# Kernel optimization log

Measured on AMD Instinct MI355X. Metric: run time of the kernel, lower is better.

Reference implementation:

```python
import jax, jax.numpy as jnp
import numpy as np

B, N_SIDE, S = 64, 40, 512
N = N_SIDE * N_SIDE          # 1600 grid points (fl_feature_dims [1,40,40])
EMB = 10                     # embedding_dim
GDIM = 8                     # lie('homography').dim
WIDTH = 128
C1 = 20                      # first-layer output channels


def _embed(x, emb_dim):
    # sinusoidal embedding of each scalar coordinate: [..., D] -> [..., D*emb_dim]
    freqs = 2.0 ** jnp.arange(emb_dim // 2, dtype=x.dtype)
    ang = x[..., None] * freqs                       # [..., D, emb/2]
    e = jnp.concatenate([jnp.sin(ang), jnp.cos(ang)], axis=-1)  # [..., D, emb]
    return e.reshape(x.shape[:-1] + (x.shape[-1] * emb_dim,))


def _glorot(key, shape):
    fan_in = shape[0]
    return jax.random.normal(key, shape, dtype=jnp.float32) / np.sqrt(fan_in)


def setup_inputs() -> dict:
    key = jax.random.key(0)
    ks = jax.random.split(key, 16)
    inp = {
        'data':   jax.random.normal(ks[0], (B, N, 1), dtype=jnp.float32),
        'v0':     jax.random.normal(ks[1], (S, GDIM), dtype=jnp.float32),
        'v_last': jax.random.normal(ks[2], (S, GDIM), dtype=jnp.float32),
        # FirstLayer filter MLP: 2*EMB -> 20 -> 20 -> 1*C1
        'fl_w1': _glorot(ks[3], (2 * EMB, 20)), 'fl_b1': jnp.zeros((20,), jnp.float32),
        'fl_w2': _glorot(ks[4], (20, 20)),      'fl_b2': jnp.zeros((20,), jnp.float32),
        'fl_w3': _glorot(ks[5], (20, C1)),      'fl_b3': jnp.zeros((C1,), jnp.float32),
        # Hidden FilterMLP: EMB*GDIM=80 -> WIDTH -> C1*WIDTH
        's_w1': _glorot(ks[6], (EMB * GDIM, WIDTH)), 's_b1': jnp.zeros((WIDTH,), jnp.float32),
        's_w2': _glorot(ks[7], (WIDTH, C1 * WIDTH)), 's_b2': jnp.zeros((C1 * WIDTH,), jnp.float32),
        'fc1_w': _glorot(ks[8], (WIDTH, WIDTH)), 'fc1_b': jnp.zeros((WIDTH,), jnp.float32),
        'fc2_w': _glorot(ks[9], (WIDTH, WIDTH)), 'fc2_b': jnp.zeros((WIDTH,), jnp.float32),
        'pool_w': _glorot(ks[10], (WIDTH, 10)),  'pool_b': jnp.zeros((10,), jnp.float32),
    }
    return inp


def reference(data, v0, v_last, fl_w1, fl_b1, fl_w2, fl_b2, fl_w3, fl_b3,
              s_w1, s_b1, s_w2, s_b2, fc1_w, fc1_b, fc2_w, fc2_b, pool_w, pool_b):
    silu = jax.nn.silu
    # pixel grid in [-1,1]^2, homogeneous coords [N,3]
    lin = jnp.linspace(-1.0, 1.0, N_SIDE, dtype=data.dtype)
    xx, yy = jnp.meshgrid(lin, lin, indexing='ij')
    coords = jnp.stack([xx.ravel(), yy.ravel()], axis=-1)           # [N,2]
    xh = jnp.concatenate([coords, jnp.ones((N, 1), data.dtype)], -1)  # [N,3]
    # homography matrices: identity + small perturbation from 8 group params
    pert = jnp.concatenate([0.1 * v_last, jnp.zeros((S, 1), data.dtype)], -1).reshape(S, 3, 3)
    H = jnp.eye(3, dtype=data.dtype) + pert                          # [S,3,3]
    y = jnp.einsum('sij,nj->sni', H, xh)                             # [S,N,3]
    t = y[..., :2] / y[..., 2:3]                                     # projective action [S,N,2]
    # continuous-kernel first layer: filters generated by MLP on embedded coords
    e1 = _embed(t, EMB)                                              # [S,N,20]
    h = silu(e1 @ fl_w1 + fl_b1)
    h = silu(h @ fl_w2 + fl_b2)
    filt1 = h @ fl_w3 + fl_b3                                        # [S,N,C1]
    z = jnp.einsum('bn,sno->bso', data[:, :, 0], filt1) / N          # [B,S,C1]
    z = silu(z)
    # hidden FilterMLP on group samples v0 -> per-sample filters [S,C1,WIDTH]
    v0e = _embed(v0, EMB)                                            # [S,80]
    h2 = silu(v0e @ s_w1 + s_b1)                                     # [S,WIDTH]
    filt2 = (h2 @ s_w2 + s_b2).reshape(S, C1, WIDTH)
    # (1/S) * sum over group-sample and channel axes of broadcast product
    z = jnp.einsum('bsc,scw->bw', z, filt2) / S                      # [B,WIDTH]
    z = silu(z @ fc1_w + fc1_b) + z
    z = silu(z @ fc2_w + fc2_b) + z
    return z @ pool_w + pool_b                                       # [B,10]
```

## Files before the change

kernel.cpp:

```cpp
#include <hip/hip_runtime.h>

#define N_PTS 1600
#define NSIDE 40
#define SNUM  512
#define BNUM  64
#define C1D   20
#define WID   128

typedef _Float16 h8  __attribute__((ext_vector_type(8)));
typedef _Float16 h4  __attribute__((ext_vector_type(4)));
typedef __fp16   h2v __attribute__((ext_vector_type(2)));
typedef float    f4  __attribute__((ext_vector_type(4)));

__device__ __forceinline__ float silu_f(float x){
    return x * __builtin_amdgcn_rcpf(1.f + __expf(-x));
}
__device__ __forceinline__ void fma4(float4& a, float s, const float4 w){
    a.x += s*w.x; a.y += s*w.y; a.z += s*w.z; a.w += s*w.w;
}

__global__ __launch_bounds__(256) void ka_prep(
    const float* __restrict__ data, const float* __restrict__ v0,
    const float* __restrict__ s_w1, const float* __restrict__ s_b1,
    const float* __restrict__ s_w2, const float* __restrict__ s_b2,
    const float* __restrict__ w1, const float* __restrict__ b1,
    const float* __restrict__ w2, const float* __restrict__ b2,
    const float* __restrict__ w3, const float* __restrict__ b3,
    _Float16* __restrict__ dataA, float* __restrict__ f2g,
    _Float16* __restrict__ wPackA, float* __restrict__ bPackA,
    float* __restrict__ out2g)
{
    const int t  = threadIdx.x;
    const int bx = blockIdx.x;
    if (bx == 370) {
        const float* wsrc[3] = { w1, w2, w3 };
        const float* bsrc[3] = { b1, b2, b3 };
        for (int v = t; v < 3072; v += 256) {
            const int l = v >> 10, rem = v & 1023;
            const int cout = rem >> 5, cin = rem & 31;
            float x = 0.f;
            if (cout < 20 && cin < 20) x = wsrc[l][cin * 20 + cout];
            wPackA[v] = (_Float16)x;
        }
        if (t < 96) {
            const int l = t >> 5, cout = t & 31;
            bPackA[t] = (cout < 20) ? bsrc[l][cout] : 0.f;
        }
        for (int v = t; v < 8192; v += 256) out2g[v] = 0.f;
        return;
    }
    if (bx >= 320) {
        const int o  = (bx - 320) * 256 + t;
        const int L  = o & 63, cm = o >> 6;
        const int mt = cm & 3, ch = cm >> 2;
        const int b  = mt * 16 + (L & 15);
        const int nb = ch * 32 + (L >> 4) * 8;
        const float* src = data + b * N_PTS + nb;
        h8 v;
        #pragma unroll
        for (int j = 0; j < 8; j++) v[j] = (_Float16)src[j];
        *(h8*)(dataA + (size_t)o * 8) = v;
        return;
    }
    const int st  = bx / 10, ct = bx - st * 10;
    const int s0  = st * 16;
    const int col = ct * 256 + t;
    __shared__ __align__(16) float h2t[128][20];

    for (int idx = t; idx < 2048; idx += 256) {
        const int ss = idx >> 7, j = idx & 127;
        float acc = s_b1[j];
        #pragma unroll
        for (int d = 0; d < 8; d++) {
            const float val = v0[(s0 + ss) * 8 + d];
            float sv, cv;
            __sincosf(val, &sv, &cv);
            #pragma unroll
            for (int k = 0; k < 5; k++) {
                acc += sv * s_w1[(d*10 + k)     * WID + j];
                acc += cv * s_w1[(d*10 + 5 + k) * WID + j];
                const float ns = 2.f * sv * cv;
                const float nc = 1.f - 2.f * sv * sv;
                sv = ns; cv = nc;
            }
        }
        h2t[j][ss] = silu_f(acc);
    }
    __syncthreads();

    float4 acc[4];
    #pragma unroll
    for (int qq = 0; qq < 4; qq++) acc[qq] = make_float4(0.f, 0.f, 0.f, 0.f);
    #pragma unroll 4
    for (int i = 0; i < 128; i++) {
        const float wv = s_w2[i * 2560 + col];
        const float4* hh = (const float4*)&h2t[i][0];
        #pragma unroll
        for (int qq = 0; qq < 4; qq++) fma4(acc[qq], wv, hh[qq]);
    }
    const float bias = s_b2[col];
    const float* af = (const float*)acc;
    #pragma unroll
    for (int ss = 0; ss < 16; ss++)
        f2g[(s0 + ss) * 2560 + col] = af[ss] + bias;
}

__device__ __forceinline__ void embed_pt(int n, const float Hm[9], h2v e2[10])
{
    const int i = n / NSIDE;
    const int j = n - i * NSIDE;
    const float x = -1.f + (float)i * (2.f/39.f);
    const float y = -1.f + (float)j * (2.f/39.f);
    const float y0 = Hm[0]*x + Hm[1]*y + Hm[2];
    const float y1 = Hm[3]*x + Hm[4]*y + Hm[5];
    const float y2 = Hm[6]*x + Hm[7]*y + Hm[8];
    const float inv = __builtin_amdgcn_rcpf(y2);
    const float t0 = y0 * inv, t1 = y1 * inv;
    float e[20];
    float sv0, cv0, sv1, cv1;
    __sincosf(t0, &sv0, &cv0);
    __sincosf(t1, &sv1, &cv1);
    #pragma unroll
    for (int k = 0; k < 5; k++) {
        e[k] = sv0; e[5+k] = cv0; e[10+k] = sv1; e[15+k] = cv1;
        const float ns0 = 2.f*sv0*cv0, nc0 = 1.f - 2.f*sv0*sv0; sv0 = ns0; cv0 = nc0;
        const float ns1 = 2.f*sv1*cv1, nc1 = 1.f - 2.f*sv1*sv1; sv1 = ns1; cv1 = nc1;
    }
    #pragma unroll
    for (int k = 0; k < 10; k++)
        e2[k] = __builtin_amdgcn_cvt_pkrtz(e[2*k], e[2*k+1]);
}

#define ASTRIDE 40

__global__ __launch_bounds__(512, 8) void k1_filt_z(
    const _Float16* __restrict__ dataA, const float* __restrict__ v_last,
    const _Float16* __restrict__ wPackA, const float* __restrict__ bPackA,
    float* __restrict__ zpart)
{
    const int s    = blockIdx.x & 511;
    const int half = blockIdx.x >> 9;
    const int nb0  = half * 800;
    const int t    = threadIdx.x;
    const int lane = t & 63;
    const int w    = t >> 6;
    const int q    = lane >> 4;
    const int l15  = lane & 15;
    const int mtbase = (w & 1) * 2;
    const int kcs    = w >> 1;

    __shared__ __align__(16) unsigned char pool[21504];
    __shared__ __align__(16) _Float16 filtB[20 * 264];
    __shared__ __align__(16) _Float16 wlds[3072];
    __shared__ __align__(16) float    blds[96];
    _Float16* act = (_Float16*)pool;
    float*    red = (float*)pool;

    for (int v = t; v < 1536; v += 512)
        ((unsigned int*)wlds)[v] = ((const unsigned int*)wPackA)[v];
    if (t < 96) blds[t] = bPackA[t];

    float Hm[9];
    #pragma unroll
    for (int k = 0; k < 9; k++) Hm[k] = (k == 0 || k == 4 || k == 8) ? 1.f : 0.f;
    #pragma unroll
    for (int k = 0; k < 8; k++) Hm[k] += 0.1f * v_last[s*8 + k];

    f4 zacc[2][2];
    #pragma unroll
    for (int mi = 0; mi < 2; mi++) { zacc[mi][0] = (f4)(0.f); zacc[mi][1] = (f4)(0.f); }
    const f4 zero4 = (f4)(0.f);

    if (t < 256) {
        unsigned long long* pz = (unsigned long long*)(act + t*ASTRIDE + 20);
        pz[0] = 0ull; pz[1] = 0ull; pz[2] = 0ull;
    }

    for (int base = 0; base < 800; base += 256) {
        const int tn = min(256, 800 - base);
        if (t < tn) {
            h2v e2[10];
            embed_pt(nb0 + base + t, Hm, e2);
            #pragma unroll
            for (int k = 0; k < 10; k++)
                *(h2v*)(act + t*ASTRIDE + 2*k) = e2[k];
        }
        __syncthreads();

        const int nmt = tn >> 4;
        #pragma unroll
        for (int l = 0; l < 3; l++) {
            const h8 wf0 = *(const h8*)(wlds + ((l*2+0)*16 + l15) * 32 + q*8);
            const h8 wf1 = *(const h8*)(wlds + ((l*2+1)*16 + l15) * 32 + q*8);
            const float b0 = blds[(l*2+0)*16 + l15];
            const float b1 = blds[(l*2+1)*16 + l15];
            for (int mt = w; mt < nmt; mt += 8) {
                const int r0 = mt * 16;
                const h8 af = *(const h8*)(act + (r0 + l15)*ASTRIDE + q*8);
                f4 D0 = __builtin_amdgcn_mfma_f32_16x16x32_f16(af, wf0, zero4, 0, 0, 0);
                f4 D1 = __builtin_amdgcn_mfma_f32_16x16x32_f16(af, wf1, zero4, 0, 0, 0);
                if (l < 2) {
                    #pragma unroll
                    for (int r = 0; r < 4; r++) {
                        const int p = r0 + q*4 + r;
                        act[p*ASTRIDE + l15] = (_Float16)silu_f(D0[r] + b0);
                        if (l15 < 4)
                            act[p*ASTRIDE + 16 + l15] = (_Float16)silu_f(D1[r] + b1);
                    }
                } else {
                    h4 p0, p1;
                    #pragma unroll
                    for (int r = 0; r < 4; r++) {
                        p0[r] = (_Float16)(D0[r] + b0);
                        p1[r] = (_Float16)(D1[r] + b1);
                    }
                    *(h4*)(filtB + l15*264 + r0 + q*4) = p0;
                    if (l15 < 4)
                        *(h4*)(filtB + (16 + l15)*264 + r0 + q*4) = p1;
                }
            }
        }
        __syncthreads();

        const int nkc = tn >> 5;
        const int r1row = (l15 < 4) ? (16 + l15) : 0;
        #pragma unroll
        for (int kk = 0; kk < 2; kk++) {
            const int kc = kcs + kk*4;
            if (kc < nkc) {
                const int gchunk = ((nb0 + base) >> 5) + kc;
                const h8 bf0 = *(const h8*)(filtB + l15  *264 + kc*32 + q*8);
                const h8 bf1 = *(const h8*)(filtB + r1row*264 + kc*32 + q*8);
                #pragma unroll
                for (int mi = 0; mi < 2; mi++) {
                    const int mt = mtbase + mi;
                    const h8 afz = *(const h8*)(dataA + ((size_t)(gchunk*4 + mt)*64 + lane)*8);
                    zacc[mi][0] = __builtin_amdgcn_mfma_f32_16x16x32_f16(afz, bf0, zacc[mi][0], 0, 0, 0);
                    zacc[mi][1] = __builtin_amdgcn_mfma_f32_16x16x32_f16(afz, bf1, zacc[mi][1], 0, 0, 0);
                }
            }
        }
        __syncthreads();
    }

    #pragma unroll
    for (int mi = 0; mi < 2; mi++) {
        #pragma unroll
        for (int r = 0; r < 4; r++) {
            const int bl = mi*16 + q*4 + r;
            red[(w*32 + bl)*21 + l15] = zacc[mi][0][r];
            if (l15 < 4) red[(w*32 + bl)*21 + 16 + l15] = zacc[mi][1][r];
        }
    }
    __syncthreads();
    for (int v = t; v < 1280; v += 512) {
        const int c = v >> 6, b = v & 63;
        const int mts = b >> 5, bl = b & 31;
        const float sum = red[((mts    )*32 + bl)*21 + c]
                        + red[((mts + 2)*32 + bl)*21 + c]
                        + red[((mts + 4)*32 + bl)*21 + c]
                        + red[((mts + 6)*32 + bl)*21 + c];
        zpart[(half*512 + s)*1280 + v] = sum;
    }
}

__global__ __launch_bounds__(256) void k2_contract(
    const float* __restrict__ zg, const float* __restrict__ f2g,
    float* __restrict__ out2g)
{
    const int blk = blockIdx.x;
    const int sg  = blk >> 1;
    const int wh  = blk & 1;
    const int s0  = sg * 4;
    const int w0  = wh * 64;
    const int t   = threadIdx.x;
    __shared__ __align__(16) float zl[4*1280];
    __shared__ __align__(16) float fl[4*20*64];
    #pragma unroll
    for (int sp = 0; sp < 4; sp++) {
        const int srow = (s0 + sp) * 1280;
        for (int r = t; r < 1280; r += 256) {
            const float a0 = zg[srow + r];
            const float a1 = zg[512*1280 + srow + r];
            zl[sp*1280 + r] = silu_f((a0 + a1) * (1.f / (float)N_PTS));
        }
        for (int u = t; u < 1280; u += 256) {
            const int c = u >> 6, ww = u & 63;
            fl[sp*1280 + u] = f2g[(s0 + sp)*2560 + c*128 + w0 + ww];
        }
    }
    __syncthreads();
    const int ww = t & 63, bh = t >> 6;
    float4 acc[4];
    #pragma unroll
    for (int qq = 0; qq < 4; qq++) acc[qq] = make_float4(0.f, 0.f, 0.f, 0.f);
    #pragma unroll 4
    for (int sc = 0; sc < 80; sc++) {
        const float f = fl[sc * 64 + ww];
        const float4* zz = (const float4*)&zl[sc * 64 + bh * 16];
        #pragma unroll
        for (int qq = 0; qq < 4; qq++) fma4(acc[qq], f, zz[qq]);
    }
    const float* af = (const float*)acc;
    #pragma unroll
    for (int idx = 0; idx < 16; idx++) {
        const int b = bh * 16 + idx;
        atomicAdd(&out2g[b * 128 + w0 + ww], af[idx]);
    }
}

__global__ __launch_bounds__(128) void k3_tail(
    const float* __restrict__ out2g,
    const float* __restrict__ fc1w, const float* __restrict__ fc1b,
    const float* __restrict__ fc2w, const float* __restrict__ fc2b,
    const float* __restrict__ pw,   const float* __restrict__ pb,
    float* __restrict__ out)
{
    const int b = blockIdx.x, t = threadIdx.x;
    __shared__ float zb[128], r1[128], r2[128];
    zb[t] = out2g[b * 128 + t] * (1.f / (float)SNUM);
    __syncthreads();
    float a = fc1b[t];
    #pragma unroll 8
    for (int i = 0; i < 128; i++) a += zb[i] * fc1w[i * 128 + t];
    r1[t] = silu_f(a) + zb[t];
    __syncthreads();
    a = fc2b[t];
    #pragma unroll 8
    for (int i = 0; i < 128; i++) a += r1[i] * fc2w[i * 128 + t];
    r2[t] = silu_f(a) + r1[t];
    __syncthreads();
    if (t < 10) {
        float o = pb[t];
        #pragma unroll 8
        for (int i = 0; i < 128; i++) o += r2[i] * pw[i * 10 + t];
        out[b * 10 + t] = o;
    }
}

extern "C" void kernel_launch(void* const* d_in, const int* in_sizes, int n_in,
                              void* d_out, int out_size, void* d_ws, size_t ws_size,
                              hipStream_t stream) {
    const float* data   = (const float*)d_in[0];
    const float* v0     = (const float*)d_in[1];
    const float* v_last = (const float*)d_in[2];
    const float* fl_w1  = (const float*)d_in[3];
    const float* fl_b1  = (const float*)d_in[4];
    const float* fl_w2  = (const float*)d_in[5];
    const float* fl_b2  = (const float*)d_in[6];
    const float* fl_w3  = (const float*)d_in[7];
    const float* fl_b3  = (const float*)d_in[8];
    const float* s_w1   = (const float*)d_in[9];
    const float* s_b1   = (const float*)d_in[10];
    const float* s_w2   = (const float*)d_in[11];
    const float* s_b2   = (const float*)d_in[12];
    const float* fc1_w  = (const float*)d_in[13];
    const float* fc1_b  = (const float*)d_in[14];
    const float* fc2_w  = (const float*)d_in[15];
    const float* fc2_b  = (const float*)d_in[16];
    const float* pool_w = (const float*)d_in[17];
    const float* pool_b = (const float*)d_in[18];
    float* out = (float*)d_out;

    float* ws        = (float*)d_ws;
    _Float16* dataA  = (_Float16*)ws;
    float* zpart  = ws    + 51200;
    float* f2g    = zpart + 1310720;
    float* out2g  = f2g   + 1310720;
    _Float16* wPackA = (_Float16*)(out2g + 8192);
    float* bPackA = out2g + 8192 + 1536;

    ka_prep    <<<371, 256, 0, stream>>>(data, v0, s_w1, s_b1, s_w2, s_b2,
                                         fl_w1, fl_b1, fl_w2, fl_b2, fl_w3, fl_b3,
                                         dataA, f2g, wPackA, bPackA, out2g);
    k1_filt_z  <<<1024, 512, 0, stream>>>(dataA, v_last, wPackA, bPackA, zpart);
    k2_contract<<<256, 256, 0, stream>>>(zpart, f2g, out2g);
    k3_tail    <<<64, 128, 0, stream>>>(out2g, fc1_w, fc1_b, fc2_w, fc2_b,
                                        pool_w, pool_b, out);
}
```

Baseline: 181.3 us.

## Split point embedding across all threads and share sincos in filter prep

```diff
diff --git a/kernel.cpp b/kernel.cpp
--- a/kernel.cpp
+++ b/kernel.cpp
@@ -66,25 +66,42 @@
     const int s0  = st * 16;
     const int col = ct * 256 + t;
     __shared__ __align__(16) float h2t[128][20];
-
-    for (int idx = t; idx < 2048; idx += 256) {
-        const int ss = idx >> 7, j = idx & 127;
-        float acc = s_b1[j];
-        #pragma unroll
+    __shared__ __align__(16) float svt[16][8][10];
+
+    if (t < 128) {
+        const int ss = t >> 3, d = t & 7;
+        const float val = v0[(s0 + ss) * 8 + d];
+        float sv, cv;
+        __sincosf(val, &sv, &cv);
+        #pragma unroll
+        for (int k = 0; k < 5; k++) {
+            svt[ss][d][k]     = sv;
+            svt[ss][d][5 + k] = cv;
+            const float ns = 2.f * sv * cv;
+            const float nc = 1.f - 2.f * sv * sv;
+            sv = ns; cv = nc;
+        }
+    }
+    __syncthreads();
+
+    {
+        const int j  = t & 127;
+        const int sh = t >> 7;
+        float hacc[8];
+        const float bias1 = s_b1[j];
+        #pragma unroll
+        for (int u = 0; u < 8; u++) hacc[u] = bias1;
         for (int d = 0; d < 8; d++) {
-            const float val = v0[(s0 + ss) * 8 + d];
-            float sv, cv;
-            __sincosf(val, &sv, &cv);
             #pragma unroll
-            for (int k = 0; k < 5; k++) {
-                acc += sv * s_w1[(d*10 + k)     * WID + j];
-                acc += cv * s_w1[(d*10 + 5 + k) * WID + j];
-                const float ns = 2.f * sv * cv;
-                const float nc = 1.f - 2.f * sv * sv;
-                sv = ns; cv = nc;
+            for (int kk = 0; kk < 10; kk++) {
+                const float wv = s_w1[(d * 10 + kk) * WID + j];
+                #pragma unroll
+                for (int u = 0; u < 8; u++)
+                    hacc[u] += svt[sh * 8 + u][d][kk] * wv;
             }
         }
-        h2t[j][ss] = silu_f(acc);
+        #pragma unroll
+        for (int u = 0; u < 8; u++) h2t[j][sh * 8 + u] = silu_f(hacc[u]);
     }
     __syncthreads();
 
@@ -105,30 +122,28 @@
         f2g[(s0 + ss) * 2560 + col] = af[ss] + bias;
 }
 
-__device__ __forceinline__ void embed_pt(int n, const float Hm[9], h2v e2[10])
+__device__ __forceinline__ void embed_coord(
+    int n, float hA, float hB, float hC, float h6, float h7, float h8c,
+    h2v e5[5])
 {
     const int i = n / NSIDE;
     const int j = n - i * NSIDE;
     const float x = -1.f + (float)i * (2.f/39.f);
     const float y = -1.f + (float)j * (2.f/39.f);
-    const float y0 = Hm[0]*x + Hm[1]*y + Hm[2];
-    const float y1 = Hm[3]*x + Hm[4]*y + Hm[5];
-    const float y2 = Hm[6]*x + Hm[7]*y + Hm[8];
-    const float inv = __builtin_amdgcn_rcpf(y2);
-    const float t0 = y0 * inv, t1 = y1 * inv;
-    float e[20];
-    float sv0, cv0, sv1, cv1;
-    __sincosf(t0, &sv0, &cv0);
-    __sincosf(t1, &sv1, &cv1);
+    const float yc = hA*x + hB*y + hC;
+    const float y2 = h6*x + h7*y + h8c;
+    const float tc = yc * __builtin_amdgcn_rcpf(y2);
+    float e[10];
+    float sv, cv;
+    __sincosf(tc, &sv, &cv);
     #pragma unroll
     for (int k = 0; k < 5; k++) {
-        e[k] = sv0; e[5+k] = cv0; e[10+k] = sv1; e[15+k] = cv1;
-        const float ns0 = 2.f*sv0*cv0, nc0 = 1.f - 2.f*sv0*sv0; sv0 = ns0; cv0 = nc0;
-        const float ns1 = 2.f*sv1*cv1, nc1 = 1.f - 2.f*sv1*sv1; sv1 = ns1; cv1 = nc1;
-    }
-    #pragma unroll
-    for (int k = 0; k < 10; k++)
-        e2[k] = __builtin_amdgcn_cvt_pkrtz(e[2*k], e[2*k+1]);
+        e[k] = sv; e[5+k] = cv;
+        const float ns = 2.f*sv*cv, nc = 1.f - 2.f*sv*sv; sv = ns; cv = nc;
+    }
+    #pragma unroll
+    for (int k = 0; k < 5; k++)
+        e5[k] = __builtin_amdgcn_cvt_pkrtz(e[2*k], e[2*k+1]);
 }
 
 #define ASTRIDE 40
@@ -148,6 +163,9 @@
     const int l15  = lane & 15;
     const int mtbase = (w & 1) * 2;
     const int kcs    = w >> 1;
+    const int ep   = lane >> 1;
+    const int ec   = lane & 1;
+    const int erow = w*16 + ep + ((ep >> 4) * 112);
 
     __shared__ __align__(16) unsigned char pool[21504];
     __shared__ __align__(16) _Float16 filtB[20 * 264];
@@ -165,27 +183,32 @@
     for (int k = 0; k < 9; k++) Hm[k] = (k == 0 || k == 4 || k == 8) ? 1.f : 0.f;
     #pragma unroll
     for (int k = 0; k < 8; k++) Hm[k] += 0.1f * v_last[s*8 + k];
+    const float hA = ec ? Hm[3] : Hm[0];
+    const float hB = ec ? Hm[4] : Hm[1];
+    const float hC = ec ? Hm[5] : Hm[2];
 
     f4 zacc[2][2];
     #pragma unroll
     for (int mi = 0; mi < 2; mi++) { zacc[mi][0] = (f4)(0.f); zacc[mi][1] = (f4)(0.f); }
     const f4 zero4 = (f4)(0.f);
 
-    if (t < 256) {
-        unsigned long long* pz = (unsigned long long*)(act + t*ASTRIDE + 20);
+    if (ec == 0) {
+        unsigned long long* pz = (unsigned long long*)(act + erow*ASTRIDE + 20);
         pz[0] = 0ull; pz[1] = 0ull; pz[2] = 0ull;
     }
+
+    __syncthreads();
 
     for (int base = 0; base < 800; base += 256) {
         const int tn = min(256, 800 - base);
-        if (t < tn) {
-            h2v e2[10];
-            embed_pt(nb0 + base + t, Hm, e2);
+
+        if (erow < tn) {
+            h2v e5[5];
+            embed_coord(nb0 + base + erow, hA, hB, hC, Hm[6], Hm[7], Hm[8], e5);
             #pragma unroll
-            for (int k = 0; k < 10; k++)
-                *(h2v*)(act + t*ASTRIDE + 2*k) = e2[k];
-        }
-        __syncthreads();
+            for (int k = 0; k < 5; k++)
+                *(h2v*)(act + erow*ASTRIDE + ec*10 + 2*k) = e5[k];
+        }
 
         const int nmt = tn >> 4;
         #pragma unroll
```

New measurement: 181.7 us. No clear change (+0.2%).
